# Optimization experiments

Hardware: AMD Instinct MI355X
Metric: run time of the kernel (lower is better)

The kernel has to match this reference:

```python
import jax, jax.numpy as jnp
import numpy as np

N = 100000      # nodes
E = 1600000     # edges
FX = 128        # raw node feature dim
MAXZ = 100      # z embedding / one-hot size
HID = 128       # hidden_channels
NL = 3          # num_layers
G = 512         # num graphs
BN_EPS = 1e-5


def _lin(key, din, dout):
    return jax.random.normal(key, (din, dout), jnp.float32) * (1.0 / np.sqrt(din))


def setup_inputs() -> dict:
    key = jax.random.key(0)
    ks = jax.random.split(key, 64)
    d = {}
    d["x"] = jax.random.normal(ks[0], (N, FX), jnp.float32)
    d["z"] = jax.random.randint(ks[1], (N,), 0, MAXZ)
    d["edge_index"] = jax.random.randint(ks[2], (2, E), 0, N)
    d["batch"] = jnp.sort(jax.random.randint(ks[3], (N,), 0, G))
    in0 = FX + 2 * MAXZ  # z_emb concatenated twice (faithful to source)
    ki = 4
    for l in range(NL):
        din = in0 if l == 0 else HID
        d[f"W1_{l}"] = _lin(ks[ki], din, HID); ki += 1
        d[f"b1_{l}"] = jnp.zeros((HID,), jnp.float32)
        d[f"W2_{l}"] = _lin(ks[ki], HID, HID); ki += 1
        d[f"b2_{l}"] = jnp.zeros((HID,), jnp.float32)
        d[f"g_{l}"] = jnp.ones((HID,), jnp.float32)
        d[f"be_{l}"] = jnp.zeros((HID,), jnp.float32)
    d["Wl1"] = _lin(ks[ki], NL * HID, HID); ki += 1
    d["bl1"] = jnp.zeros((HID,), jnp.float32)
    d["Wl2"] = _lin(ks[ki], HID, 1); ki += 1
    d["bl2"] = jnp.zeros((1,), jnp.float32)
    return d


def _gin_layer(h, src, dst, W1, b1, W2, b2, g, be):
    # GINConv with eps=0: nn(x + sum_{j->i} x_j)
    agg = jax.ops.segment_sum(h[src], dst, num_segments=N)  # [N, d]
    m = h + agg
    m = jax.nn.relu(m @ W1 + b1)
    m = jax.nn.relu(m @ W2 + b2)
    # training-mode BatchNorm1d over node axis (biased variance)
    mu = m.mean(0)
    var = jnp.mean((m - mu) ** 2, axis=0)
    return (m - mu) * jax.lax.rsqrt(var + BN_EPS) * g + be


def reference(x, z, edge_index, batch,
              W1_0, b1_0, W2_0, b2_0, g_0, be_0,
              W1_1, b1_1, W2_1, b2_1, g_1, be_1,
              W1_2, b1_2, W2_2, b2_2, g_2, be_2,
              Wl1, bl1, Wl2, bl2):
    src, dst = edge_index[0], edge_index[1]
    z_emb = jax.nn.one_hot(z, MAXZ, dtype=jnp.float32)  # [N, MAXZ]
    h = jnp.concatenate([z_emb, x], axis=1)
    h = jnp.concatenate([z_emb, h], axis=1)  # faithful double concat -> [N, FX+2*MAXZ]
    params = [(W1_0, b1_0, W2_0, b2_0, g_0, be_0),
              (W1_1, b1_1, W2_1, b2_1, g_1, be_1),
              (W1_2, b1_2, W2_2, b2_2, g_2, be_2)]
    xs = []
    for p in params:
        h = _gin_layer(h, src, dst, *p)
        xs.append(h)
    hcat = jnp.concatenate(xs, axis=1)  # jumping knowledge: [N, NL*HID]
    # global_mean_pool over graph ids
    counts = jax.ops.segment_sum(jnp.ones((N,), jnp.float32), batch, num_segments=G)
    pooled = jax.ops.segment_sum(hcat, batch, num_segments=G) / jnp.maximum(counts, 1.0)[:, None]
    out = jax.nn.relu(pooled @ Wl1 + bl1)
    # dropout is identity in eval / reference mode
    out = out @ Wl2 + bl2  # [G, 1]
    return out
```

## Files before the change

kernel.cpp:

```cpp
#include <hip/hip_runtime.h>
#include <hip/hip_bf16.h>

#define NN 100000
#define NROWS_PAD 100032
#define EE 1600000
#define GG 512
#define SCAN_CHUNK 512
#define SCAN_BLOCKS ((NN + SCAN_CHUNK - 1) / SCAN_CHUNK)
#define NPB 256
#define NB  ((NN + NPB - 1) / NPB)
#define PCHUNK 4096
#define PBLOCKS ((EE + PCHUNK - 1) / PCHUNK)
static constexpr float BN_EPS = 1e-5f;

typedef _Float16 half8 __attribute__((ext_vector_type(8)));
typedef _Float16 half4 __attribute__((ext_vector_type(4)));
typedef float floatx4 __attribute__((ext_vector_type(4)));


__global__ __launch_bounds__(256) void k_bhist(const int* __restrict__ EI,
                                               int* __restrict__ bcount)
{
    __shared__ int h[NB];
    const int t = threadIdx.x;
    for (int i = t; i < NB; i += 256) h[i] = 0;
    __syncthreads();
    const int e0 = blockIdx.x * PCHUNK;
    const int e1 = (e0 + PCHUNK < EE) ? e0 + PCHUNK : EE;
    for (int e = e0 + t; e < e1; e += 256)
        atomicAdd(&h[EI[EE + e] >> 8], 1);
    __syncthreads();
    for (int i = t; i < NB; i += 256)
        if (h[i]) atomicAdd(&bcount[i], h[i]);
}

__global__ __launch_bounds__(512) void k_bscan(const int* __restrict__ bcount,
                                               int* __restrict__ bstart,
                                               int* __restrict__ bcursor)
{
    __shared__ int s[512];
    int t = threadIdx.x;
    int v = (t < NB) ? bcount[t] : 0;
    s[t] = v;
    __syncthreads();
    for (int off = 1; off < 512; off <<= 1) {
        int u = (t >= off) ? s[t - off] : 0;
        __syncthreads();
        s[t] += u;
        __syncthreads();
    }
    if (t < NB) { int ex = s[t] - v; bstart[t] = ex; bcursor[t] = ex; }
    if (t == 0) bstart[NB] = EE;
}

__global__ __launch_bounds__(256) void k_part(const int* __restrict__ EI,
                                              int* __restrict__ bcursor,
                                              int* __restrict__ ebuf)
{
    __shared__ int h[NB];
    __shared__ int cur[NB];
    const int t = threadIdx.x;
    for (int i = t; i < NB; i += 256) h[i] = 0;
    __syncthreads();
    const int e0 = blockIdx.x * PCHUNK;
    const int e1 = (e0 + PCHUNK < EE) ? e0 + PCHUNK : EE;
    for (int e = e0 + t; e < e1; e += 256)
        atomicAdd(&h[EI[EE + e] >> 8], 1);
    __syncthreads();
    for (int i = t; i < NB; i += 256)
        cur[i] = h[i] ? atomicAdd(&bcursor[i], h[i]) : 0;
    __syncthreads();
    for (int e = e0 + t; e < e1; e += 256) {
        int s = EI[e], d = EI[EE + e];
        int pos = atomicAdd(&cur[d >> 8], 1);
        ebuf[pos] = s | ((d & (NPB - 1)) << 17);
    }
}

__global__ __launch_bounds__(256) void k_nhist(const int* __restrict__ ebuf,
                                               const int* __restrict__ bstart,
                                               int* __restrict__ hist)
{
    __shared__ int cnt[NPB];
    const int b = blockIdx.x, t = threadIdx.x;
    cnt[t] = 0;
    __syncthreads();
    const int e0 = bstart[b], e1 = bstart[b + 1];
    for (int e = e0 + t; e < e1; e += 256) {
        unsigned p = (unsigned)__builtin_nontemporal_load(&ebuf[e]);
        atomicAdd(&cnt[p >> 17], 1);
    }
    __syncthreads();
    int idx = b * NPB + t;
    if (idx < NN) hist[idx] = cnt[t];
}

__global__ __launch_bounds__(256) void k_scan1(const int* __restrict__ hist,
                                               int* __restrict__ partials)
{
    __shared__ int red[256];
    int b = blockIdx.x, t = threadIdx.x;
    int i0 = b * SCAN_CHUNK + 2 * t;
    int e0 = (i0 < NN) ? hist[i0] : 0;
    int e1 = (i0 + 1 < NN) ? hist[i0 + 1] : 0;
    red[t] = e0 + e1;
    __syncthreads();
    for (int off = 128; off > 0; off >>= 1) {
        if (t < off) red[t] += red[t + off];
        __syncthreads();
    }
    if (t == 0) partials[b] = red[0];
}

__global__ __launch_bounds__(256) void k_scan2(const int* __restrict__ partials,
                                               int* __restrict__ poffs,
                                               int* __restrict__ row_start)
{
    __shared__ int s[256];
    int t = threadIdx.x;
    int v = (t < SCAN_BLOCKS) ? partials[t] : 0;
    s[t] = v;
    __syncthreads();
    for (int off = 1; off < 256; off <<= 1) {
        int u = (t >= off) ? s[t - off] : 0;
        __syncthreads();
        s[t] += u;
        __syncthreads();
    }
    if (t < SCAN_BLOCKS) poffs[t] = s[t] - v;
    if (t == 0) row_start[NN] = EE;
}

__global__ __launch_bounds__(256) void k_scan3(const int* __restrict__ hist,
                                               const int* __restrict__ poffs,
                                               int* __restrict__ row_start)
{
    __shared__ int s[256];
    int b = blockIdx.x, t = threadIdx.x;
    int i0 = b * SCAN_CHUNK + 2 * t;
    int e0 = (i0 < NN) ? hist[i0] : 0;
    int e1 = (i0 + 1 < NN) ? hist[i0 + 1] : 0;
    int pair = e0 + e1;
    s[t] = pair;
    __syncthreads();
    for (int off = 1; off < 256; off <<= 1) {
        int u = (t >= off) ? s[t - off] : 0;
        __syncthreads();
        s[t] += u;
        __syncthreads();
    }
    int base = poffs[b] + s[t] - pair;
    if (i0 < NN)     row_start[i0] = base;
    if (i0 + 1 < NN) row_start[i0 + 1] = base + e0;
}

__global__ __launch_bounds__(256) void k_fill2(const int* __restrict__ ebuf,
                                               const int* __restrict__ bstart,
                                               const int* __restrict__ row_start,
                                               int* __restrict__ ssrc)
{
    __shared__ int cur[NPB];
    const int b = blockIdx.x, t = threadIdx.x;
    int idx = b * NPB + t;
    cur[t] = (idx < NN) ? row_start[idx] : 0;
    __syncthreads();
    const int e0 = bstart[b], e1 = bstart[b + 1];
    for (int e = e0 + t; e < e1; e += 256) {
        unsigned p = (unsigned)__builtin_nontemporal_load(&ebuf[e]);
        int pos = atomicAdd(&cur[p >> 17], 1);
        ssrc[pos] = (int)(p & 0x1FFFFu);
    }
}


__global__ __launch_bounds__(256) void k_xcast(const float* __restrict__ X,
                                               _Float16* __restrict__ Xh)
{
    int idx = blockIdx.x * 256 + threadIdx.x;
    const float4* src = (const float4*)X;
    float4 a = src[idx * 2], b = src[idx * 2 + 1];
    half8 o = { (_Float16)a.x, (_Float16)a.y, (_Float16)a.z, (_Float16)a.w,
                (_Float16)b.x, (_Float16)b.y, (_Float16)b.z, (_Float16)b.w };
    *(half8*)&Xh[idx * 8] = o;
}

__global__ __launch_bounds__(256) void k_prep(
    const float* __restrict__ W1, const float* __restrict__ W2,
    const float* __restrict__ scale, const float* __restrict__ shift,
    _Float16* __restrict__ Wt1, _Float16* __restrict__ Wt2,
    float* __restrict__ cvec, int l)
{
    int b = blockIdx.x, t = threadIdx.x;
    if (b < 64) {
        int idx = b * 256 + t;
        int n = idx >> 7, k = idx & 127;
        Wt1[idx] = (l == 0) ? (_Float16)W1[(200 + k) * 128 + n]
                            : (_Float16)(scale[k] * W1[k * 128 + n]);
    } else if (b < 128) {
        int idx = (b - 64) * 256 + t;
        int n = idx >> 7, k = idx & 127;
        Wt2[idx] = (_Float16)W2[k * 128 + n];
    } else if (t < 128) {
        float acc = 0.f;
        if (l != 0)
            for (int k = 0; k < 128; ++k) acc = fmaf(shift[k], W1[k * 128 + t], acc);
        cvec[t] = acc;
    }
}


#define MM_PREAMBLE(Wth)                                                     \
    __shared__ _Float16 Wl[128][136];                                        \
    const int tid = threadIdx.x;                                             \
    const int row0 = blockIdx.x * 64;                                        \
    {                                                                        \
        for (int it = 0; it < 8; ++it) {                                     \
            int idx = tid + it * 256;                                        \
            int r = idx >> 4, seg = idx & 15;                                \
            *(half8*)&Wl[r][seg * 8] = *(const half8*)&Wth[r * 128 + seg * 8];\
        }                                                                    \
    }

#define MM_CORE(Ah)                                                          \
    const int lane = tid & 63;                                               \
    const int wv = tid >> 6;                                                 \
    const int ml = lane & 15;                                                \
    const int quad = lane >> 4;                                              \
    const int wr = wv >> 1, wc = wv & 1;                                     \
    floatx4 acc[2][4];                                                       \
    for (int r = 0; r < 2; ++r)                                              \
        for (int t = 0; t < 4; ++t)                                          \
            acc[r][t] = (floatx4){0.f, 0.f, 0.f, 0.f};                       \
    {                                                                        \
        const size_t ar0 = (size_t)(row0 + 32 * wr + ml) * 128;              \
        const size_t ar1 = ar0 + (size_t)16 * 128;                           \
        _Pragma("unroll")                                                    \
        for (int kq = 0; kq < 4; ++kq) {                                     \
            int k0 = kq * 32;                                                \
            half8 a0 = *(const half8*)&Ah[ar0 + k0 + quad * 8];              \
            half8 a1 = *(const half8*)&Ah[ar1 + k0 + quad * 8];              \
            _Pragma("unroll")                                                \
            for (int t = 0; t < 4; ++t) {                                    \
                half8 bf = *(const half8*)&Wl[64 * wc + 16 * t + ml][k0 + quad * 8]; \
                acc[0][t] = __builtin_amdgcn_mfma_f32_16x16x32_f16(a0, bf, acc[0][t], 0, 0, 0); \
                acc[1][t] = __builtin_amdgcn_mfma_f32_16x16x32_f16(a1, bf, acc[1][t], 0, 0, 0); \
            }                                                                \
        }                                                                    \
    }

__global__ __launch_bounds__(256) void k_mm_embed(
    const _Float16* __restrict__ Ah, const _Float16* __restrict__ Wth,
    const int* __restrict__ Z, const float* __restrict__ W1,
    _Float16* __restrict__ Ph)
{
    MM_PREAMBLE(Wth)
    __syncthreads();
    MM_CORE(Ah)
    #pragma unroll
    for (int r = 0; r < 2; ++r)
        #pragma unroll
        for (int j = 0; j < 4; ++j) {
            int grow = row0 + 32 * wr + 16 * r + quad * 4 + j;
            if (grow < NN) {
                int zv = Z[grow];
                const float* w0 = &W1[zv * 128];
                const float* w1 = &W1[(100 + zv) * 128];
                #pragma unroll
                for (int t = 0; t < 4; ++t) {
                    int gcol = 64 * wc + 16 * t + ml;
                    float v = acc[r][t][j] + w0[gcol] + w1[gcol];
                    Ph[(size_t)grow * 128 + gcol] = (_Float16)v;
                }
            }
        }
}

__global__ __launch_bounds__(256) void k_mm1(
    const _Float16* __restrict__ Ah, const _Float16* __restrict__ Wth,
    _Float16* __restrict__ Ph)
{
    MM_PREAMBLE(Wth)
    __syncthreads();
    MM_CORE(Ah)
    #pragma unroll
    for (int r = 0; r < 2; ++r)
        #pragma unroll
        for (int j = 0; j < 4; ++j) {
            int grow = row0 + 32 * wr + 16 * r + quad * 4 + j;
            if (grow < NN) {
                #pragma unroll
                for (int t = 0; t < 4; ++t) {
                    int gcol = 64 * wc + 16 * t + ml;
                    Ph[(size_t)grow * 128 + gcol] = (_Float16)acc[r][t][j];
                }
            }
        }
}

__global__ __launch_bounds__(256) void k_mm2(
    const _Float16* __restrict__ Ah, const _Float16* __restrict__ Wth,
    const float* __restrict__ b2, _Float16* __restrict__ Oh,
    float* __restrict__ colsum, float* __restrict__ colsq)
{
    __shared__ float cs[128];
    __shared__ float cq[128];
    MM_PREAMBLE(Wth)
    if (tid < 128) { cs[tid] = 0.f; cq[tid] = 0.f; }
    __syncthreads();
    MM_CORE(Ah)
    float b2v[4];
    #pragma unroll
    for (int t = 0; t < 4; ++t) b2v[t] = b2[64 * wc + 16 * t + ml];
    float st[4] = {0.f, 0.f, 0.f, 0.f};
    float qt[4] = {0.f, 0.f, 0.f, 0.f};
    #pragma unroll
    for (int r = 0; r < 2; ++r)
        #pragma unroll
        for (int j = 0; j < 4; ++j) {
            int grow = row0 + 32 * wr + 16 * r + quad * 4 + j;
            if (grow < NN) {
                #pragma unroll
                for (int t = 0; t < 4; ++t) {
                    int gcol = 64 * wc + 16 * t + ml;
                    float v = fmaxf(acc[r][t][j] + b2v[t], 0.f);
                    Oh[(size_t)grow * 128 + gcol] = (_Float16)v;
                    st[t] += v;
                    qt[t] += v * v;
                }
            }
        }
    #pragma unroll
    for (int t = 0; t < 4; ++t) {
        int gcol = 64 * wc + 16 * t + ml;
        atomicAdd(&cs[gcol], st[t]);
        atomicAdd(&cq[gcol], qt[t]);
    }
    __syncthreads();
    if (tid < 128) {
        atomicAdd(&colsum[tid], cs[tid]);
        atomicAdd(&colsq[tid], cq[tid]);
    }
}


__global__ __launch_bounds__(256) void k_aggregate(
    const _Float16* __restrict__ Ph, const int* __restrict__ row_start,
    const int* __restrict__ ssrc, const float* __restrict__ b1,
    const float* __restrict__ cvec, _Float16* __restrict__ Mh)
{
    int idx = blockIdx.x * 256 + threadIdx.x;
    int node = idx >> 4, q = idx & 15;
    if (node >= NN) return;
    int s0 = row_start[node], s1 = row_start[node + 1];
    float degp1 = (float)(s1 - s0 + 1);
    float acc[8];
    half8 pv = *(const half8*)&Ph[(size_t)node * 128 + q * 8];
    #pragma unroll
    for (int j = 0; j < 8; ++j)
        acc[j] = (float)pv[j] + fmaf(degp1, cvec[q * 8 + j], b1[q * 8 + j]);
    int e = s0;
    for (; e + 3 < s1; e += 4) {
        int sa = __builtin_nontemporal_load(&ssrc[e]);
        int sb = __builtin_nontemporal_load(&ssrc[e + 1]);
        int sc = __builtin_nontemporal_load(&ssrc[e + 2]);
        int sd = __builtin_nontemporal_load(&ssrc[e + 3]);
        half8 va = *(const half8*)&Ph[(size_t)sa * 128 + q * 8];
        half8 vb = *(const half8*)&Ph[(size_t)sb * 128 + q * 8];
        half8 vc = *(const half8*)&Ph[(size_t)sc * 128 + q * 8];
        half8 vd = *(const half8*)&Ph[(size_t)sd * 128 + q * 8];
        #pragma unroll
        for (int j = 0; j < 8; ++j)
            acc[j] += ((float)va[j] + (float)vb[j]) + ((float)vc[j] + (float)vd[j]);
    }
    for (; e < s1; ++e) {
        int sa = __builtin_nontemporal_load(&ssrc[e]);
        half8 va = *(const half8*)&Ph[(size_t)sa * 128 + q * 8];
        #pragma unroll
        for (int j = 0; j < 8; ++j) acc[j] += (float)va[j];
    }
    half8 o;
    #pragma unroll
    for (int j = 0; j < 8; ++j) o[j] = (_Float16)fmaxf(acc[j], 0.f);
    __builtin_nontemporal_store(o, (half8*)&Mh[(size_t)node * 128 + q * 8]);
}

__global__ void k_bnfin(const float* __restrict__ colsum, const float* __restrict__ colsq,
                        const float* __restrict__ g, const float* __restrict__ be,
                        float* __restrict__ scale, float* __restrict__ shift)
{
    int c = threadIdx.x;
    float inv_n = 1.0f / (float)NN;
    float mu = colsum[c] * inv_n;
    float var = colsq[c] * inv_n - mu * mu;
    float sc = g[c] * rsqrtf(var + BN_EPS);
    scale[c] = sc;
    shift[c] = be[c] - mu * sc;
}

__global__ __launch_bounds__(128) void k_pool(
    const _Float16* __restrict__ Ah, const int* __restrict__ batch,
    const float* __restrict__ scale, const float* __restrict__ shift,
    float* __restrict__ pooled, int loff)
{
    __shared__ float red[8][128];
    int g = blockIdx.x;
    int t = threadIdx.x;
    int rg = t >> 4, seg = t & 15;
    int lo = 0, hi = NN;
    while (lo < hi) { int mid = (lo + hi) >> 1; if (batch[mid] < g) lo = mid + 1; else hi = mid; }
    int s = lo;
    lo = s; hi = NN;
    while (lo < hi) { int mid = (lo + hi) >> 1; if (batch[mid] < g + 1) lo = mid + 1; else hi = mid; }
    int e = lo;
    float acc[8] = {};
    for (int i = s + rg; i < e; i += 8) {
        half8 v = *(const half8*)&Ah[(size_t)i * 128 + seg * 8];
        #pragma unroll
        for (int j = 0; j < 8; ++j) acc[j] += (float)v[j];
    }
    #pragma unroll
    for (int j = 0; j < 8; ++j) red[rg][seg * 8 + j] = acc[j];
    __syncthreads();
    int cnt = e - s;
    float inv = 1.0f / (float)(cnt > 0 ? cnt : 1);
    if (t < 128) {
        float s_ = 0.f;
        #pragma unroll
        for (int r = 0; r < 8; ++r) s_ += red[r][t];
        pooled[g * 384 + loff + t] = fmaf(scale[t], s_ * inv, shift[t]);
    }
}

__global__ __launch_bounds__(128) void k_final(
    const float* __restrict__ pooled,
    const float* __restrict__ Wl1, const float* __restrict__ bl1,
    const float* __restrict__ Wl2, const float* __restrict__ bl2,
    float* __restrict__ out)
{
    __shared__ float pr[384];
    __shared__ float red[128];
    int g = blockIdx.x, j = threadIdx.x;
    for (int i = j; i < 384; i += 128) pr[i] = pooled[g * 384 + i];
    __syncthreads();
    float acc = bl1[j];
    for (int k = 0; k < 384; ++k) acc = fmaf(pr[k], Wl1[k * 128 + j], acc);
    float r = fmaxf(acc, 0.f) * Wl2[j];
    red[j] = r;
    __syncthreads();
    for (int off = 64; off > 0; off >>= 1) {
        if (j < off) red[j] += red[j + off];
        __syncthreads();
    }
    if (j == 0) out[g] = red[0] + bl2[0];
}

extern "C" void kernel_launch(void* const* d_in, const int* in_sizes, int n_in,
                              void* d_out, int out_size, void* d_ws, size_t ws_size,
                              hipStream_t stream)
{
    const float* x     = (const float*)d_in[0];
    const int*   z     = (const int*)d_in[1];
    const int*   ei    = (const int*)d_in[2];
    const int*   batch = (const int*)d_in[3];
    const float* W1a[3] = {(const float*)d_in[4],  (const float*)d_in[10], (const float*)d_in[16]};
    const float* b1a[3] = {(const float*)d_in[5],  (const float*)d_in[11], (const float*)d_in[17]};
    const float* W2a[3] = {(const float*)d_in[6],  (const float*)d_in[12], (const float*)d_in[18]};
    const float* b2a[3] = {(const float*)d_in[7],  (const float*)d_in[13], (const float*)d_in[19]};
    const float* ga[3]  = {(const float*)d_in[8],  (const float*)d_in[14], (const float*)d_in[20]};
    const float* bea[3] = {(const float*)d_in[9],  (const float*)d_in[15], (const float*)d_in[21]};
    const float* Wl1 = (const float*)d_in[22];
    const float* bl1 = (const float*)d_in[23];
    const float* Wl2 = (const float*)d_in[24];
    const float* bl2 = (const float*)d_in[25];
    float* out = (float*)d_out;

    char* ws = (char*)d_ws;
    size_t off = 0;
    auto alloc = [&](size_t bytes) {
        void* p = ws + off;
        off += (bytes + 255) & ~(size_t)255;
        return p;
    };
    _Float16* Xh  = (_Float16*)alloc((size_t)NROWS_PAD * 128 * 2);
    _Float16* Ph  = (_Float16*)alloc((size_t)NROWS_PAD * 128 * 2);
    _Float16* Mh  = (_Float16*)alloc((size_t)NROWS_PAD * 128 * 2);
    _Float16* Ahb = (_Float16*)alloc((size_t)NROWS_PAD * 128 * 2);
    _Float16* Wt1 = (_Float16*)alloc((size_t)128 * 128 * 2);
    _Float16* Wt2 = (_Float16*)alloc((size_t)128 * 128 * 2);
    int*   ebuf     = (int*)alloc((size_t)EE * 4);
    int*   ssrc     = (int*)alloc((size_t)EE * 4);
    int*   hist     = (int*)alloc((size_t)NN * 4);
    int*   row_st   = (int*)alloc((size_t)(NN + 1) * 4);
    int*   bcount   = (int*)alloc((size_t)NB * 4);
    int*   bstart   = (int*)alloc((size_t)(NB + 1) * 4);
    int*   bcursor  = (int*)alloc((size_t)NB * 4);
    int*   partials = (int*)alloc((size_t)SCAN_BLOCKS * 4);
    int*   poffs    = (int*)alloc((size_t)SCAN_BLOCKS * 4);
    float* cvec     = (float*)alloc(128 * 4);
    float* stats    = (float*)alloc(3 * 256 * 4);
    float* scale    = (float*)alloc(128 * 4);
    float* shift    = (float*)alloc(128 * 4);
    float* pooled   = (float*)alloc((size_t)GG * 384 * 4);

    const int gemmBlocks = (NN + 63) / 64;
    const int aggBlocks  = (NN * 16 + 255) / 256;

    hipMemsetAsync(stats, 0, 3 * 256 * 4, stream);
    hipMemsetAsync(bcount, 0, (size_t)NB * 4, stream);
    k_xcast<<<(NN * 128 / 8 + 255) / 256, 256, 0, stream>>>(x, Xh);
    k_bhist<<<PBLOCKS, 256, 0, stream>>>(ei, bcount);
    k_bscan<<<1, 512, 0, stream>>>(bcount, bstart, bcursor);
    k_part<<<PBLOCKS, 256, 0, stream>>>(ei, bcursor, ebuf);
    k_nhist<<<NB, 256, 0, stream>>>(ebuf, bstart, hist);
    k_scan1<<<SCAN_BLOCKS, 256, 0, stream>>>(hist, partials);
    k_scan2<<<1, 256, 0, stream>>>(partials, poffs, row_st);
    k_scan3<<<SCAN_BLOCKS, 256, 0, stream>>>(hist, poffs, row_st);
    k_fill2<<<NB, 256, 0, stream>>>(ebuf, bstart, row_st, ssrc);

    for (int l = 0; l < 3; ++l) {
        float* colsum = stats + l * 256;
        float* colsq  = stats + l * 256 + 128;
        k_prep<<<129, 256, 0, stream>>>(W1a[l], W2a[l], scale, shift, Wt1, Wt2, cvec, l);
        if (l == 0)
            k_mm_embed<<<gemmBlocks, 256, 0, stream>>>(Xh, Wt1, z, W1a[0], Ph);
        else
            k_mm1<<<gemmBlocks, 256, 0, stream>>>(Ahb, Wt1, Ph);
        k_aggregate<<<aggBlocks, 256, 0, stream>>>(Ph, row_st, ssrc, b1a[l], cvec, Mh);
        k_mm2<<<gemmBlocks, 256, 0, stream>>>(Mh, Wt2, b2a[l], Ahb, colsum, colsq);
        k_bnfin<<<1, 128, 0, stream>>>(colsum, colsq, ga[l], bea[l], scale, shift);
        k_pool<<<GG, 128, 0, stream>>>(Ahb, batch, scale, shift, pooled, l * 128);
    }
    k_final<<<GG, 128, 0, stream>>>(pooled, Wl1, bl1, Wl2, bl2, out);
}
```

Baseline: 713.5 us.

## Fuse CSR scan into bucket fill, pooling into mm2, drop BN and pool kernels

Several changes land together. The node-histogram, three-kernel scan and fill kernels are merged into one per-bucket kernel that scans counts in shared memory and scatters edges. Global mean pooling moves into the mm2 epilogue through shared and global atomics, with BN scale and shift applied later in the final kernel, which removes the k_bnfin and k_pool kernels. The GEMMs stop staging the weights in LDS and read B fragments straight from global memory. This cuts launches and the extra pass over activations, at the cost of many atomics in the mm2 epilogue and uncached global weight reads in the GEMM inner loop.

```diff
diff --git a/kernel.cpp b/kernel.cpp
--- a/kernel.cpp
+++ b/kernel.cpp
@@ -5,8 +5,6 @@
 #define NROWS_PAD 100032
 #define EE 1600000
 #define GG 512
-#define SCAN_CHUNK 512
-#define SCAN_BLOCKS ((NN + SCAN_CHUNK - 1) / SCAN_CHUNK)
 #define NPB 256
 #define NB  ((NN + NPB - 1) / NPB)
 #define PCHUNK 4096
@@ -14,7 +12,6 @@
 static constexpr float BN_EPS = 1e-5f;
 
 typedef _Float16 half8 __attribute__((ext_vector_type(8)));
-typedef _Float16 half4 __attribute__((ext_vector_type(4)));
 typedef float floatx4 __attribute__((ext_vector_type(4)));
 
 
@@ -36,7 +33,8 @@
 
 __global__ __launch_bounds__(512) void k_bscan(const int* __restrict__ bcount,
                                                int* __restrict__ bstart,
-                                               int* __restrict__ bcursor)
+                                               int* __restrict__ bcursor,
+                                               int* __restrict__ row_start)
 {
     __shared__ int s[512];
     int t = threadIdx.x;
@@ -50,7 +48,7 @@
         __syncthreads();
     }
     if (t < NB) { int ex = s[t] - v; bstart[t] = ex; bcursor[t] = ex; }
-    if (t == 0) bstart[NB] = EE;
+    if (t == 0) { bstart[NB] = EE; row_start[NN] = EE; }
 }
 
 __global__ __launch_bounds__(256) void k_part(const int* __restrict__ EI,
@@ -77,11 +75,13 @@
     }
 }
 
-__global__ __launch_bounds__(256) void k_nhist(const int* __restrict__ ebuf,
-                                               const int* __restrict__ bstart,
-                                               int* __restrict__ hist)
+__global__ __launch_bounds__(256) void k_csrbucket(const int* __restrict__ ebuf,
+                                                   const int* __restrict__ bstart,
+                                                   int* __restrict__ row_start,
+                                                   int* __restrict__ ssrc)
 {
     __shared__ int cnt[NPB];
+    __shared__ int cur[NPB];
     const int b = blockIdx.x, t = threadIdx.x;
     cnt[t] = 0;
     __syncthreads();
@@ -91,80 +91,18 @@
         atomicAdd(&cnt[p >> 17], 1);
     }
     __syncthreads();
+    int myc = cnt[t];
+    for (int off = 1; off < 256; off <<= 1) {
+        int u = (t >= off) ? cnt[t - off] : 0;
+        __syncthreads();
+        cnt[t] += u;
+        __syncthreads();
+    }
+    int pos0 = e0 + cnt[t] - myc;
     int idx = b * NPB + t;
-    if (idx < NN) hist[idx] = cnt[t];
-}
-
-__global__ __launch_bounds__(256) void k_scan1(const int* __restrict__ hist,
-                                               int* __restrict__ partials)
-{
-    __shared__ int red[256];
-    int b = blockIdx.x, t = threadIdx.x;
-    int i0 = b * SCAN_CHUNK + 2 * t;
-    int e0 = (i0 < NN) ? hist[i0] : 0;
-    int e1 = (i0 + 1 < NN) ? hist[i0 + 1] : 0;
-    red[t] = e0 + e1;
-    __syncthreads();
-    for (int off = 128; off > 0; off >>= 1) {
-        if (t < off) red[t] += red[t + off];
-        __syncthreads();
-    }
-    if (t == 0) partials[b] = red[0];
-}
-
-__global__ __launch_bounds__(256) void k_scan2(const int* __restrict__ partials,
-                                               int* __restrict__ poffs,
-                                               int* __restrict__ row_start)
-{
-    __shared__ int s[256];
-    int t = threadIdx.x;
-    int v = (t < SCAN_BLOCKS) ? partials[t] : 0;
-    s[t] = v;
-    __syncthreads();
-    for (int off = 1; off < 256; off <<= 1) {
-        int u = (t >= off) ? s[t - off] : 0;
-        __syncthreads();
-        s[t] += u;
-        __syncthreads();
-    }
-    if (t < SCAN_BLOCKS) poffs[t] = s[t] - v;
-    if (t == 0) row_start[NN] = EE;
-}
-
-__global__ __launch_bounds__(256) void k_scan3(const int* __restrict__ hist,
-                                               const int* __restrict__ poffs,
-                                               int* __restrict__ row_start)
-{
-    __shared__ int s[256];
-    int b = blockIdx.x, t = threadIdx.x;
-    int i0 = b * SCAN_CHUNK + 2 * t;
-    int e0 = (i0 < NN) ? hist[i0] : 0;
-    int e1 = (i0 + 1 < NN) ? hist[i0 + 1] : 0;
-    int pair = e0 + e1;
-    s[t] = pair;
-    __syncthreads();
-    for (int off = 1; off < 256; off <<= 1) {
-        int u = (t >= off) ? s[t - off] : 0;
-        __syncthreads();
-        s[t] += u;
-        __syncthreads();
-    }
-    int base = poffs[b] + s[t] - pair;
-    if (i0 < NN)     row_start[i0] = base;
-    if (i0 + 1 < NN) row_start[i0 + 1] = base + e0;
-}
-
-__global__ __launch_bounds__(256) void k_fill2(const int* __restrict__ ebuf,
-                                               const int* __restrict__ bstart,
-                                               const int* __restrict__ row_start,
-                                               int* __restrict__ ssrc)
-{
-    __shared__ int cur[NPB];
-    const int b = blockIdx.x, t = threadIdx.x;
-    int idx = b * NPB + t;
-    cur[t] = (idx < NN) ? row_start[idx] : 0;
-    __syncthreads();
-    const int e0 = bstart[b], e1 = bstart[b + 1];
+    if (idx < NN) row_start[idx] = pos0;
+    cur[t] = pos0;
+    __syncthreads();
     for (int e = e0 + t; e < e1; e += 256) {
         unsigned p = (unsigned)__builtin_nontemporal_load(&ebuf[e]);
         int pos = atomicAdd(&cur[p >> 17], 1);
@@ -184,9 +122,21 @@
     *(half8*)&Xh[idx * 8] = o;
 }
 
+__device__ __forceinline__ void bn_sc_sh(const float* colsum, const float* colsq,
+                                         const float* g, const float* be, int k,
+                                         float& sc, float& sh)
+{
+    float inv_n = 1.0f / (float)NN;
+    float mu = colsum[k] * inv_n;
+    float var = colsq[k] * inv_n - mu * mu;
+    sc = g[k] * rsqrtf(var + BN_EPS);
+    sh = be[k] - mu * sc;
+}
+
 __global__ __launch_bounds__(256) void k_prep(
     const float* __restrict__ W1, const float* __restrict__ W2,
-    const float* __restrict__ scale, const float* __restrict__ shift,
+    const float* __restrict__ colsum, const float* __restrict__ colsq,
+    const float* __restrict__ g, const float* __restrict__ be,
     _Float16* __restrict__ Wt1, _Float16* __restrict__ Wt2,
     float* __restrict__ cvec, int l)
 {
@@ -194,34 +144,32 @@
     if (b < 64) {
         int idx = b * 256 + t;
         int n = idx >> 7, k = idx & 127;
-        Wt1[idx] = (l == 0) ? (_Float16)W1[(200 + k) * 128 + n]
-                            : (_Float16)(scale[k] * W1[k * 128 + n]);
+        if (l == 0) {
+            Wt1[idx] = (_Float16)W1[(200 + k) * 128 + n];
+        } else {
+            float sc, sh;
+            bn_sc_sh(colsum, colsq, g, be, k, sc, sh);
+            Wt1[idx] = (_Float16)(sc * W1[k * 128 + n]);
+        }
     } else if (b < 128) {
         int idx = (b - 64) * 256 + t;
         int n = idx >> 7, k = idx & 127;
         Wt2[idx] = (_Float16)W2[k * 128 + n];
     } else if (t < 128) {
         float acc = 0.f;
-        if (l != 0)
-            for (int k = 0; k < 128; ++k) acc = fmaf(shift[k], W1[k * 128 + t], acc);
+        if (l != 0) {
+            for (int k = 0; k < 128; ++k) {
+                float sc, sh;
+                bn_sc_sh(colsum, colsq, g, be, k, sc, sh);
+                acc = fmaf(sh, W1[k * 128 + t], acc);
+            }
+        }
         cvec[t] = acc;
     }
 }
 
 
-#define MM_PREAMBLE(Wth)                                                     \
-    __shared__ _Float16 Wl[128][136];                                        \
-    const int tid = threadIdx.x;                                             \
-    const int row0 = blockIdx.x * 64;                                        \
-    {                                                                        \
-        for (int it = 0; it < 8; ++it) {                                     \
-            int idx = tid + it * 256;                                        \
-            int r = idx >> 4, seg = idx & 15;                                \
-            *(half8*)&Wl[r][seg * 8] = *(const half8*)&Wth[r * 128 + seg * 8];\
-        }                                                                    \
-    }
-
-#define MM_CORE(Ah)                                                          \
+#define MM_CORE_G(Ah, Wth)                                                   \
     const int lane = tid & 63;                                               \
     const int wv = tid >> 6;                                                 \
     const int ml = lane & 15;                                                \
@@ -241,7 +189,7 @@
             half8 a1 = *(const half8*)&Ah[ar1 + k0 + quad * 8];              \
             _Pragma("unroll")                                                \
             for (int t = 0; t < 4; ++t) {                                    \
-                half8 bf = *(const half8*)&Wl[64 * wc + 16 * t + ml][k0 + quad * 8]; \
+                half8 bf = *(const half8*)&Wth[(size_t)(64 * wc + 16 * t + ml) * 128 + k0 + quad * 8]; \
                 acc[0][t] = __builtin_amdgcn_mfma_f32_16x16x32_f16(a0, bf, acc[0][t], 0, 0, 0); \
                 acc[1][t] = __builtin_amdgcn_mfma_f32_16x16x32_f16(a1, bf, acc[1][t], 0, 0, 0); \
             }                                                                \
@@ -253,9 +201,9 @@
     const int* __restrict__ Z, const float* __restrict__ W1,
     _Float16* __restrict__ Ph)
 {
-    MM_PREAMBLE(Wth)
-    __syncthreads();
-    MM_CORE(Ah)
+    const int tid = threadIdx.x;
+    const int row0 = blockIdx.x * 64;
+    MM_CORE_G(Ah, Wth)
     #pragma unroll
     for (int r = 0; r < 2; ++r)
         #pragma unroll
@@ -279,9 +227,9 @@
     const _Float16* __restrict__ Ah, const _Float16* __restrict__ Wth,
     _Float16* __restrict__ Ph)
 {
-    MM_PREAMBLE(Wth)
-    __syncthreads();
-    MM_CORE(Ah)
+    const int tid = threadIdx.x;
+    const int row0 = blockIdx.x * 64;
+    MM_CORE_G(Ah, Wth)
     #pragma unroll
     for (int r = 0; r < 2; ++r)
         #pragma unroll
@@ -299,15 +247,25 @@
 
 __global__ __launch_bounds__(256) void k_mm2(
     const _Float16* __restrict__ Ah, const _Float16* __restrict__ Wth,
-    const float* __restrict__ b2, _Float16* __restrict__ Oh,
-    float* __restrict__ colsum, float* __restrict__ colsq)
+    const float* __restrict__ b2, const int* __restrict__ batch,
+    _Float16* __restrict__ Oh,
+    float* __restrict__ colsum, float* __restrict__ colsq,
+    float* __restrict__ gpool)
 {
     __shared__ float cs[128];
     __shared__ float cq[128];
-    MM_PREAMBLE(Wth)
-    if (tid < 128) { cs[tid] = 0.f; cq[tid] = 0.f; }
-    __syncthreads();
-    MM_CORE(Ah)
+    __shared__ float gp[8][128];
+    const int tid = threadIdx.x;
+    const int row0 = blockIdx.x * 64;
+    for (int i = tid; i < 128; i += 256) { cs[i] = 0.f; cq[i] = 0.f; }
+    for (int i = tid; i < 8 * 128; i += 256) (&gp[0][0])[i] = 0.f;
+    __syncthreads();
+
+    MM_CORE_G(Ah, Wth)
+
+    const int gmin = batch[row0];
+    const int rlast = (row0 + 63 < NN) ? row0 + 63 : NN - 1;
+    const int span = batch[rlast] - gmin;
     float b2v[4];
     #pragma unroll
     for (int t = 0; t < 4; ++t) b2v[t] = b2[64 * wc + 16 * t + ml];
@@ -319,6 +277,7 @@
         for (int j = 0; j < 4; ++j) {
             int grow = row0 + 32 * wr + 16 * r + quad * 4 + j;
             if (grow < NN) {
+                int rel = batch[grow] - gmin;
                 #pragma unroll
                 for (int t = 0; t < 4; ++t) {
                     int gcol = 64 * wc + 16 * t + ml;
@@ -326,6 +285,8 @@
                     Oh[(size_t)grow * 128 + gcol] = (_Float16)v;
                     st[t] += v;
                     qt[t] += v * v;
+                    if (rel < 8) atomicAdd(&gp[rel][gcol], v);
+                    else atomicAdd(&gpool[(size_t)batch[grow] * 128 + gcol], v);
                 }
             }
         }
@@ -339,6 +300,9 @@
     if (tid < 128) {
         atomicAdd(&colsum[tid], cs[tid]);
         atomicAdd(&colsq[tid], cq[tid]);
+        int smax = (span < 7) ? span : 7;
+        for (int rel = 0; rel <= smax; ++rel)
+            atomicAdd(&gpool[(size_t)(gmin + rel) * 128 + tid], gp[rel][tid]);
     }
 }
 
@@ -384,63 +348,36 @@
     __builtin_nontemporal_store(o, (half8*)&Mh[(size_t)node * 128 + q * 8]);
 }
 
-__global__ void k_bnfin(const float* __restrict__ colsum, const float* __restrict__ colsq,
-                        const float* __restrict__ g, const float* __restrict__ be,
-                        float* __restrict__ scale, float* __restrict__ shift)
-{
-    int c = threadIdx.x;
-    float inv_n = 1.0f / (float)NN;
-    float mu = colsum[c] * inv_n;
-    float var = colsq[c] * inv_n - mu * mu;
-    float sc = g[c] * rsqrtf(var + BN_EPS);
-    scale[c] = sc;
-    shift[c] = be[c] - mu * sc;
-}
-
-__global__ __launch_bounds__(128) void k_pool(
-    const _Float16* __restrict__ Ah, const int* __restrict__ batch,
-    const float* __restrict__ scale, const float* __restrict__ shift,
-    float* __restrict__ pooled, int loff)
-{
-    __shared__ float red[8][128];
-    int g = blockIdx.x;
-    int t = threadIdx.x;
-    int rg = t >> 4, seg = t & 15;
+
+__global__ __launch_bounds__(128) void k_final(
+    const float* __restrict__ gpool, const float* __restrict__ stats,
+    const int* __restrict__ batch,
+    const float* __restrict__ g0, const float* __restrict__ be0,
+    const float* __restrict__ g1, const float* __restrict__ be1,
+    const float* __restrict__ g2, const float* __restrict__ be2,
+    const float* __restrict__ Wl1, const float* __restrict__ bl1,
+    const float* __restrict__ Wl2, const float* __restrict__ bl2,
+    float* __restrict__ out)
+{
+    __shared__ float pr[384];
+    __shared__ float red[128];
+    int g = blockIdx.x, j = threadIdx.x;
     int lo = 0, hi = NN;
     while (lo < hi) { int mid = (lo + hi) >> 1; if (batch[mid] < g) lo = mid + 1; else hi = mid; }
     int s = lo;
     lo = s; hi = NN;
     while (lo < hi) { int mid = (lo + hi) >> 1; if (batch[mid] < g + 1) lo = mid + 1; else hi = mid; }
-    int e = lo;
-    float acc[8] = {};
-    for (int i = s + rg; i < e; i += 8) {
-        half8 v = *(const half8*)&Ah[(size_t)i * 128 + seg * 8];
-        #pragma unroll
-        for (int j = 0; j < 8; ++j) acc[j] += (float)v[j];
-    }
-    #pragma unroll
-    for (int j = 0; j < 8; ++j) red[rg][seg * 8 + j] = acc[j];
-    __syncthreads();
-    int cnt = e - s;
+    int cnt = lo - s;
     float inv = 1.0f / (float)(cnt > 0 ? cnt : 1);
-    if (t < 128) {
-        float s_ = 0.f;
-        #pragma unroll
-        for (int r = 0; r < 8; ++r) s_ += red[r][t];
-        pooled[g * 384 + loff + t] = fmaf(scale[t], s_ * inv, shift[t]);
-    }
-}
-
-__global__ __launch_bounds__(128) void k_final(
-    const float* __restrict__ pooled,
-    const float* __restrict__ Wl1, const float* __restrict__ bl1,
-    const float* __restrict__ Wl2, const float* __restrict__ bl2,
-    float* __restrict__ out)
-{
-    __shared__ float pr[384];
-    __shared__ float red[128];
-    int g = blockIdx.x, j = threadIdx.x;
-    for (int i = j; i < 384; i += 128) pr[i] = pooled[g * 384 + i];
+    #pragma unroll
+    for (int l = 0; l < 3; ++l) {
+        const float* gl  = (l == 0) ? g0 : (l == 1) ? g1 : g2;
+        const float* bel = (l == 0) ? be0 : (l == 1) ? be1 : be2;
+        float sc, sh;
+        bn_sc_sh(stats + l * 256, stats + l * 256 + 128, gl, bel, j, sc, sh);
+        float gs = gpool[((size_t)l * GG + g) * 128 + j];
+        pr[l * 128 + j] = fmaf(sc, gs * inv, sh);
+    }
     __syncthreads();
     float acc = bl1[j];
     for (int k = 0; k < 384; ++k) acc = fmaf(pr[k], Wl1[k * 128 + j], acc);
@@ -489,46 +426,42 @@
     _Float16* Wt2 = (_Float16*)alloc((size_t)128 * 128 * 2);
     int*   ebuf     = (int*)alloc((size_t)EE * 4);
     int*   ssrc     = (int*)alloc((size_t)EE * 4);
-    int*   hist     = (int*)alloc((size_t)NN * 4);
     int*   row_st   = (int*)alloc((size_t)(NN + 1) * 4);
     int*   bcount   = (int*)alloc((size_t)NB * 4);
     int*   bstart   = (int*)alloc((size_t)(NB + 1) * 4);
     int*   bcursor  = (int*)alloc((size_t)NB * 4);
-    int*   partials = (int*)alloc((size_t)SCAN_BLOCKS * 4);
-    int*   poffs    = (int*)alloc((size_t)SCAN_BLOCKS * 4);
     float* cvec     = (float*)alloc(128 * 4);
     float* stats    = (float*)alloc(3 * 256 * 4);
-    float* scale    = (float*)alloc(128 * 4);
-    float* shift    = (float*)alloc(128 * 4);
-    float* pooled   = (float*)alloc((size_t)GG * 384 * 4);
-
+    float* gpool    = (float*)alloc((size_t)3 * GG * 128 * 4);
     const int gemmBlocks = (NN + 63) / 64;
     const int aggBlocks  = (NN * 16 + 255) / 256;
 
-    hipMemsetAsync(stats, 0, 3 * 256 * 4, stream);
+    hipMemsetAsync(stats, 0, 3 * 256 * 4 + (size_t)3 * GG * 128 * 4, stream);
     hipMemsetAsync(bcount, 0, (size_t)NB * 4, stream);
     k_xcast<<<(NN * 128 / 8 + 255) / 256, 256, 0, stream>>>(x, Xh);
     k_bhist<<<PBLOCKS, 256, 0, stream>>>(ei, bcount);
-    k_bscan<<<1, 512, 0, stream>>>(bcount, bstart, bcursor);
+    k_bscan<<<1, 512, 0, stream>>>(bcount, bstart, bcursor, row_st);
     k_part<<<PBLOCKS, 256, 0, stream>>>(ei, bcursor, ebuf);
-    k_nhist<<<NB, 256, 0, stream>>>(ebuf, bstart, hist);
-    k_scan1<<<SCAN_BLOCKS, 256, 0, stream>>>(hist, partials);
-    k_scan2<<<1, 256, 0, stream>>>(partials, poffs, row_st);
-    k_scan3<<<SCAN_BLOCKS, 256, 0, stream>>>(hist, poffs, row_st);
-    k_fill2<<<NB, 256, 0, stream>>>(ebuf, bstart, row_st, ssrc);
+    k_csrbucket<<<NB, 256, 0, stream>>>(ebuf, bstart, row_st, ssrc);
 
     for (int l = 0; l < 3; ++l) {
         float* colsum = stats + l * 256;
         float* colsq  = stats + l * 256 + 128;
-        k_prep<<<129, 256, 0, stream>>>(W1a[l], W2a[l], scale, shift, Wt1, Wt2, cvec, l);
+        const float* psum = (l > 0) ? stats + (l - 1) * 256 : stats;
+        const float* psq  = (l > 0) ? stats + (l - 1) * 256 + 128 : stats + 128;
+        const float* pg   = (l > 0) ? ga[l - 1] : ga[0];
+        const float* pbe  = (l > 0) ? bea[l - 1] : bea[0];
+        k_prep<<<129, 256, 0, stream>>>(W1a[l], W2a[l], psum, psq, pg, pbe,
+                                        Wt1, Wt2, cvec, l);
         if (l == 0)
             k_mm_embed<<<gemmBlocks, 256, 0, stream>>>(Xh, Wt1, z, W1a[0], Ph);
         else
             k_mm1<<<gemmBlocks, 256, 0, stream>>>(Ahb, Wt1, Ph);
         k_aggregate<<<aggBlocks, 256, 0, stream>>>(Ph, row_st, ssrc, b1a[l], cvec, Mh);
-        k_mm2<<<gemmBlocks, 256, 0, stream>>>(Mh, Wt2, b2a[l], Ahb, colsum, colsq);
-        k_bnfin<<<1, 128, 0, stream>>>(colsum, colsq, ga[l], bea[l], scale, shift);
-        k_pool<<<GG, 128, 0, stream>>>(Ahb, batch, scale, shift, pooled, l * 128);
-    }
-    k_final<<<GG, 128, 0, stream>>>(pooled, Wl1, bl1, Wl2, bl2, out);
-}
+        k_mm2<<<gemmBlocks, 256, 0, stream>>>(Mh, Wt2, b2a[l], batch, Ahb,
+                                              colsum, colsq, gpool + (size_t)l * GG * 128);
+    }
+    k_final<<<GG, 128, 0, stream>>>(gpool, stats, batch,
+                                    ga[0], bea[0], ga[1], bea[1], ga[2], bea[2],
+                                    Wl1, bl1, Wl2, bl2, out);
+}
```

Measured after the change: 830.7 us. 16.4% more time.
